# Kernel optimization log

Measured on AMD Instinct MI355X. Metric: run time of the kernel, lower is better.

## Reference

```python
import jax, jax.numpy as jnp
import numpy as np

BETA = 3.0

def setup_inputs() -> dict:
    key = jax.random.key(0)
    k1, k2 = jax.random.split(key)
    B, C = 65536, 1000
    outputs = jax.random.normal(k1, (B, C), dtype=jnp.float32)
    targets = jax.random.randint(k2, (B,), 0, C, dtype=jnp.int64)
    cost_matrix = jnp.zeros((C, C), dtype=jnp.float32)
    return {"outputs": outputs, "targets": targets, "cost_matrix": cost_matrix}

def reference(outputs, targets, cost_matrix):
    # [B, C] log-probs, single stable pass
    log_probs = jax.nn.log_softmax(outputs, axis=1)
    predicted = jnp.argmax(log_probs, axis=1)  # [B]

    # Fused scatter-add replacing the per-sample Python loop:
    # cost_matrix[t, p] += 1 for each (t, p) pair (duplicates accumulate).
    cm = cost_matrix.at[targets, predicted].add(1.0)

    # Row-normalize: cm[i] * beta / max(1, sum(cm[i]))
    row_sum = jnp.sum(cm, axis=1, keepdims=True)  # [C, 1]
    cm_norm = cm * (BETA / jnp.maximum(1.0, row_sum))

    # gather log_probs[b, targets[b]] and cm_norm[targets[b], predicted[b]]
    gather_log_probs = jnp.take_along_axis(log_probs, targets[:, None], axis=1)[:, 0]  # [B]
    gather_costs = cm_norm[targets, predicted]  # [B]

    return -jnp.mean(gather_log_probs * gather_costs)
```

## Files before the change

kernel.cpp:

```cpp
#include <hip/hip_runtime.h>
#include <math.h>

#define CLS 1000
#define VEC_PER_ROW 250
#define BETA 3.0f
#define NPART 256

__global__ __launch_bounds__(256) void softmax_pass(
    const float* __restrict__ outputs,
    const int* __restrict__ targets,
    float* __restrict__ cm,
    float* __restrict__ logp,
    int* __restrict__ pred,
    int B)
{
    const int wave = threadIdx.x >> 6;
    const int lane = threadIdx.x & 63;
    const int row  = blockIdx.x * 4 + wave;
    if (row >= B) return;

    const float4* rp = (const float4*)(outputs + (size_t)row * CLS);

    float4 r[4];
#pragma unroll
    for (int k = 0; k < 4; ++k) {
        const int j = lane + 64 * k;
        if (j < VEC_PER_ROW) {
            r[k] = rp[j];
        } else {
            r[k] = make_float4(-INFINITY, -INFINITY, -INFINITY, -INFINITY);
        }
    }

    float m = -INFINITY;
#pragma unroll
    for (int k = 0; k < 4; ++k)
        m = fmaxf(m, fmaxf(fmaxf(r[k].x, r[k].y), fmaxf(r[k].z, r[k].w)));
#pragma unroll
    for (int off = 32; off; off >>= 1)
        m = fmaxf(m, __shfl_xor(m, off));

    float S  = 0.0f;
    int  idx = 0x7fffffff;
#pragma unroll
    for (int k = 0; k < 4; ++k) {
        const int base = (lane + 64 * k) * 4;
        const float* f = (const float*)&r[k];
#pragma unroll
        for (int c = 0; c < 4; ++c) {
            const float x = f[c];
            S += __expf(x - m);
            if (x == m) idx = min(idx, base + c);
        }
    }
#pragma unroll
    for (int off = 32; off; off >>= 1) {
        S   += __shfl_xor(S, off);
        idx  = min(idx, __shfl_xor(idx, off));
    }

    if (lane == 0) {
        const int t   = targets[row];
        const float xt = outputs[(size_t)row * CLS + t];
        logp[row] = xt - m - __logf(S);
        pred[row] = idx;
        atomicAdd(&cm[(size_t)t * CLS + idx], 1.0f);
    }
}

__global__ __launch_bounds__(256) void row_scale(
    const float* __restrict__ cm,
    float* __restrict__ scale)
{
    const int wave = threadIdx.x >> 6;
    const int lane = threadIdx.x & 63;
    const int row  = blockIdx.x * 4 + wave;
    if (row >= CLS) return;

    const float4* rp = (const float4*)(cm + (size_t)row * CLS);
    float s = 0.0f;
    for (int j = lane; j < VEC_PER_ROW; j += 64) {
        const float4 v = rp[j];
        s += v.x + v.y + v.z + v.w;
    }
#pragma unroll
    for (int off = 32; off; off >>= 1) s += __shfl_xor(s, off);
    if (lane == 0) scale[row] = BETA / fmaxf(1.0f, s);
}

__global__ __launch_bounds__(256) void finalize_partial(
    const float* __restrict__ cm,
    const float* __restrict__ scale,
    const float* __restrict__ logp,
    const int* __restrict__ pred,
    const int* __restrict__ targets,
    float* __restrict__ partial,
    int B)
{
    float v = 0.0f;
    for (int i = blockIdx.x * 256 + threadIdx.x; i < B; i += NPART * 256) {
        const int t = targets[i];
        const int p = pred[i];
        v += logp[i] * cm[(size_t)t * CLS + p] * scale[t];
    }
    const int lane = threadIdx.x & 63;
    const int wave = threadIdx.x >> 6;
#pragma unroll
    for (int off = 32; off; off >>= 1) v += __shfl_xor(v, off);

    __shared__ float ssum[4];
    if (lane == 0) ssum[wave] = v;
    __syncthreads();
    if (threadIdx.x == 0)
        partial[blockIdx.x] = ssum[0] + ssum[1] + ssum[2] + ssum[3];
}

__global__ __launch_bounds__(256) void finalize_reduce(
    const float* __restrict__ partial,
    float* __restrict__ out,
    int B)
{
    float v = (threadIdx.x < NPART) ? partial[threadIdx.x] : 0.0f;
    const int lane = threadIdx.x & 63;
    const int wave = threadIdx.x >> 6;
#pragma unroll
    for (int off = 32; off; off >>= 1) v += __shfl_xor(v, off);

    __shared__ float ssum[4];
    if (lane == 0) ssum[wave] = v;
    __syncthreads();
    if (threadIdx.x == 0)
        out[0] = -(ssum[0] + ssum[1] + ssum[2] + ssum[3]) / (float)B;
}

extern "C" void kernel_launch(void* const* d_in, const int* in_sizes, int n_in,
                              void* d_out, int out_size, void* d_ws, size_t ws_size,
                              hipStream_t stream)
{
    const float* outputs     = (const float*)d_in[0];
    const int*   targets     = (const int*)d_in[1];
    const float* cost_matrix = (const float*)d_in[2];
    const int B = in_sizes[1];

    char* ws = (char*)d_ws;
    float* cm      = (float*)(ws);
    float* logp    = (float*)(ws + 4000000);
    int*   pred    = (int*)  (ws + 4000000 + (size_t)B * 4);
    float* scale   = (float*)(ws + 4000000 + (size_t)B * 8);
    float* partial = (float*)(ws + 4000000 + (size_t)B * 8 + 4096);

    hipMemcpyAsync(cm, cost_matrix, (size_t)CLS * CLS * sizeof(float),
                   hipMemcpyDeviceToDevice, stream);

    softmax_pass<<<(B + 3) / 4, 256, 0, stream>>>(outputs, targets, cm, logp, pred, B);
    row_scale<<<(CLS + 3) / 4, 256, 0, stream>>>(cm, scale);
    finalize_partial<<<NPART, 256, 0, stream>>>(cm, scale, logp, pred, targets,
                                                partial, B);
    finalize_reduce<<<1, 256, 0, stream>>>(partial, (float*)d_out, B);
}
```

Measured before the change: 360.1 us.

## Derive row sums from target counts and fuse final reduction via last-block counter

Replaces the memcpy plus separate row-sum kernel with an init kernel that copies the cost matrix and records its original row sums, while the softmax pass also counts targets per class atomically. Row normalization is then computed as the initial row sum plus the target count, which removes the second scan over the 4MB matrix. The final two-stage reduction is merged into one kernel using an atomic counter so the last block finishes the sum. In exchange it adds one more atomic per row in the main pass and relies on release/acquire ordering for the partial sums.

Measured after the change: 364.1 us. About the same (+1.1%).

```diff
diff --git a/kernel.cpp b/kernel.cpp
--- a/kernel.cpp
+++ b/kernel.cpp
@@ -6,10 +6,40 @@
 #define BETA 3.0f
 #define NPART 256
 
+__global__ __launch_bounds__(256) void cm_init(
+    const float* __restrict__ cm0,
+    float* __restrict__ cm,
+    float* __restrict__ inRowsum,
+    int* __restrict__ tcount,
+    int* __restrict__ counter)
+{
+    if (blockIdx.x == 0) {
+        for (int i = threadIdx.x; i < CLS; i += 256) tcount[i] = 0;
+        if (threadIdx.x == 0) *counter = 0;
+    }
+    const int wave = threadIdx.x >> 6;
+    const int lane = threadIdx.x & 63;
+    const int row  = blockIdx.x * 4 + wave;
+    if (row >= CLS) return;
+
+    const float4* src = (const float4*)(cm0 + (size_t)row * CLS);
+    float4*       dst = (float4*)(cm  + (size_t)row * CLS);
+    float s = 0.0f;
+    for (int j = lane; j < VEC_PER_ROW; j += 64) {
+        const float4 v = src[j];
+        dst[j] = v;
+        s += v.x + v.y + v.z + v.w;
+    }
+#pragma unroll
+    for (int off = 32; off; off >>= 1) s += __shfl_xor(s, off);
+    if (lane == 0) inRowsum[row] = s;
+}
+
 __global__ __launch_bounds__(256) void softmax_pass(
     const float* __restrict__ outputs,
     const int* __restrict__ targets,
     float* __restrict__ cm,
+    int* __restrict__ tcount,
     float* __restrict__ logp,
     int* __restrict__ pred,
     int B)
@@ -65,43 +95,28 @@
         logp[row] = xt - m - __logf(S);
         pred[row] = idx;
         atomicAdd(&cm[(size_t)t * CLS + idx], 1.0f);
+        atomicAdd(&tcount[t], 1);
     }
 }
 
-__global__ __launch_bounds__(256) void row_scale(
+__global__ __launch_bounds__(256) void finalize(
     const float* __restrict__ cm,
-    float* __restrict__ scale)
-{
-    const int wave = threadIdx.x >> 6;
-    const int lane = threadIdx.x & 63;
-    const int row  = blockIdx.x * 4 + wave;
-    if (row >= CLS) return;
-
-    const float4* rp = (const float4*)(cm + (size_t)row * CLS);
-    float s = 0.0f;
-    for (int j = lane; j < VEC_PER_ROW; j += 64) {
-        const float4 v = rp[j];
-        s += v.x + v.y + v.z + v.w;
-    }
-#pragma unroll
-    for (int off = 32; off; off >>= 1) s += __shfl_xor(s, off);
-    if (lane == 0) scale[row] = BETA / fmaxf(1.0f, s);
-}
-
-__global__ __launch_bounds__(256) void finalize_partial(
-    const float* __restrict__ cm,
-    const float* __restrict__ scale,
+    const float* __restrict__ inRowsum,
+    const int* __restrict__ tcount,
     const float* __restrict__ logp,
     const int* __restrict__ pred,
     const int* __restrict__ targets,
     float* __restrict__ partial,
+    int* __restrict__ counter,
+    float* __restrict__ out,
     int B)
 {
     float v = 0.0f;
     for (int i = blockIdx.x * 256 + threadIdx.x; i < B; i += NPART * 256) {
         const int t = targets[i];
         const int p = pred[i];
-        v += logp[i] * cm[(size_t)t * CLS + p] * scale[t];
+        const float rs = inRowsum[t] + (float)tcount[t];
+        v += logp[i] * cm[(size_t)t * CLS + p] * (BETA / fmaxf(1.0f, rs));
     }
     const int lane = threadIdx.x & 63;
     const int wave = threadIdx.x >> 6;
@@ -109,25 +124,28 @@
     for (int off = 32; off; off >>= 1) v += __shfl_xor(v, off);
 
     __shared__ float ssum[4];
+    __shared__ int lastFlag;
     if (lane == 0) ssum[wave] = v;
     __syncthreads();
-    if (threadIdx.x == 0)
-        partial[blockIdx.x] = ssum[0] + ssum[1] + ssum[2] + ssum[3];
-}
+    if (threadIdx.x == 0) {
+        const float p4 = ssum[0] + ssum[1] + ssum[2] + ssum[3];
+        __hip_atomic_store(&partial[blockIdx.x], p4,
+                           __ATOMIC_RELEASE, __HIP_MEMORY_SCOPE_AGENT);
+        const int old = __hip_atomic_fetch_add(counter, 1,
+                           __ATOMIC_ACQ_REL, __HIP_MEMORY_SCOPE_AGENT);
+        lastFlag = (old == NPART - 1);
+    }
+    __syncthreads();
+    if (!lastFlag) return;
 
-__global__ __launch_bounds__(256) void finalize_reduce(
-    const float* __restrict__ partial,
-    float* __restrict__ out,
-    int B)
-{
-    float v = (threadIdx.x < NPART) ? partial[threadIdx.x] : 0.0f;
-    const int lane = threadIdx.x & 63;
-    const int wave = threadIdx.x >> 6;
+    float w = (threadIdx.x < NPART)
+        ? __hip_atomic_load(&partial[threadIdx.x],
+                            __ATOMIC_ACQUIRE, __HIP_MEMORY_SCOPE_AGENT)
+        : 0.0f;
 #pragma unroll
-    for (int off = 32; off; off >>= 1) v += __shfl_xor(v, off);
-
-    __shared__ float ssum[4];
-    if (lane == 0) ssum[wave] = v;
+    for (int off = 32; off; off >>= 1) w += __shfl_xor(w, off);
+    __syncthreads();
+    if (lane == 0) ssum[wave] = w;
     __syncthreads();
     if (threadIdx.x == 0)
         out[0] = -(ssum[0] + ssum[1] + ssum[2] + ssum[3]) / (float)B;
@@ -143,18 +161,19 @@
     const int B = in_sizes[1];
 
     char* ws = (char*)d_ws;
-    float* cm      = (float*)(ws);
-    float* logp    = (float*)(ws + 4000000);
-    int*   pred    = (int*)  (ws + 4000000 + (size_t)B * 4);
-    float* scale   = (float*)(ws + 4000000 + (size_t)B * 8);
-    float* partial = (float*)(ws + 4000000 + (size_t)B * 8 + 4096);
+    float* cm       = (float*)(ws);
+    float* logp     = (float*)(ws + 4000000);
+    int*   pred     = (int*)  (ws + 4000000 + (size_t)B * 4);
+    float* inRowsum = (float*)(ws + 4000000 + (size_t)B * 8);
+    int*   tcount   = (int*)  (ws + 4000000 + (size_t)B * 8 + 4096);
+    float* partial  = (float*)(ws + 4000000 + (size_t)B * 8 + 8192);
+    int*   counter  = (int*)  (ws + 4000000 + (size_t)B * 8 + 9216);
 
-    hipMemcpyAsync(cm, cost_matrix, (size_t)CLS * CLS * sizeof(float),
-                   hipMemcpyDeviceToDevice, stream);
-
-    softmax_pass<<<(B + 3) / 4, 256, 0, stream>>>(outputs, targets, cm, logp, pred, B);
-    row_scale<<<(CLS + 3) / 4, 256, 0, stream>>>(cm, scale);
-    finalize_partial<<<NPART, 256, 0, stream>>>(cm, scale, logp, pred, targets,
-                                                partial, B);
-    finalize_reduce<<<1, 256, 0, stream>>>(partial, (float*)d_out, B);
+    cm_init<<<(CLS + 3) / 4, 256, 0, stream>>>(cost_matrix, cm, inRowsum,
+                                               tcount, counter);
+    softmax_pass<<<(B + 3) / 4, 256, 0, stream>>>(outputs, targets, cm, tcount,
+                                                  logp, pred, B);
+    finalize<<<NPART, 256, 0, stream>>>(cm, inRowsum, tcount, logp, pred,
+                                        targets, partial, counter,
+                                        (float*)d_out, B);
 }
```
